# Performance work log

Measured on AMD Instinct MI355X. Metric: run time of the kernel, lower is better.

The kernel has to match this reference:

```python
import jax, jax.numpy as jnp
import numpy as np

DIM = 512
NUM_HEADS = 8
HEAD_DIM = DIM // NUM_HEADS
SCALE = HEAD_DIM ** -0.5
B, N = 8, 1024


def setup_inputs() -> dict:
    key = jax.random.key(0)
    k1, k2, k3, k4, k5 = jax.random.split(key, 5)
    x = jax.random.normal(k1, (B, N, DIM), dtype=jnp.float32)
    rpe_bias = jax.random.normal(k2, (1, NUM_HEADS, N, N), dtype=jnp.float32)
    # torch Linear weights: [out_features, in_features], y = x @ W.T
    qkv_w = jax.random.normal(k3, (3 * DIM, DIM), dtype=jnp.float32) * (DIM ** -0.5)
    proj_w = jax.random.normal(k4, (DIM, DIM), dtype=jnp.float32) * (DIM ** -0.5)
    proj_b = jax.random.normal(k5, (DIM,), dtype=jnp.float32) * 0.01
    return {"x": x, "rpe_bias": rpe_bias, "qkv_w": qkv_w, "proj_w": proj_w, "proj_b": proj_b}


def reference(x, rpe_bias, qkv_w, proj_w, proj_b):
    b, n, c = x.shape
    h, d = NUM_HEADS, HEAD_DIM
    # qkv projection (no bias): [B,N,3C] -> [3,B,H,N,D]
    qkv = (x @ qkv_w.T).reshape(b, n, 3, h, d).transpose(2, 0, 3, 1, 4)
    q, k, v = qkv[0], qkv[1], qkv[2]
    attn = jnp.einsum('bhnd,bhmd->bhnm', q, k) * SCALE + rpe_bias
    attn = jax.nn.softmax(attn, axis=-1)  # dropout p=0 -> identity
    out = jnp.einsum('bhnm,bhmd->bhnd', attn, v)
    out = out.transpose(0, 2, 1, 3).reshape(b, n, c)
    return out @ proj_w.T + proj_b
```

## Files before the change

### kernel.cpp

```cpp
#include <hip/hip_runtime.h>
#include <hip/hip_bf16.h>

#define B_    8
#define N_    1024
#define DIM_  512
#define H_    8
#define DH_   64
#define SCALE_ 0.125f

typedef unsigned short u16;
typedef __attribute__((ext_vector_type(8))) short bf16x8;
typedef __attribute__((ext_vector_type(4))) float f32x4;

__device__ __forceinline__ u16 f2bf(float f) {
  union { float f; unsigned u; } v; v.f = f;
  return (u16)((v.u + 0x7fffu + ((v.u >> 16) & 1u)) >> 16);
}
__device__ __forceinline__ unsigned pack2(float a, float b) {
  return (unsigned)f2bf(a) | ((unsigned)f2bf(b) << 16);
}
__device__ __forceinline__ void cp16(const void* g, void* l) {
  __builtin_amdgcn_global_load_lds(
      (const __attribute__((address_space(1))) unsigned*)g,
      (__attribute__((address_space(3))) unsigned*)l, 16, 0, 0);
}

__global__ __launch_bounds__(256) void convert_kernel(
    const float* __restrict__ X, const float* __restrict__ Wq,
    const float* __restrict__ Wp, u16* __restrict__ Xb,
    u16* __restrict__ Wqb, u16* __restrict__ Wpb) {
  const int NX4 = (B_ * N_ * DIM_) / 4;
  const int NQ4 = (3 * DIM_ * DIM_) / 4;
  const int NP4 = (DIM_ * DIM_) / 4;
  const int total = NX4 + NQ4 + NP4;
  const int stride = gridDim.x * 256;
  for (int i = blockIdx.x * 256 + threadIdx.x; i < total; i += stride) {
    const float* s; u16* d; int off;
    if (i < NX4)            { s = X;  d = Xb;  off = i; }
    else if (i < NX4 + NQ4) { s = Wq; d = Wqb; off = i - NX4; }
    else                    { s = Wp; d = Wpb; off = i - NX4 - NQ4; }
    float4 f = *(const float4*)(s + (size_t)off * 4);
    uint2 u; u.x = pack2(f.x, f.y); u.y = pack2(f.z, f.w);
    *(uint2*)(d + (size_t)off * 4) = u;
  }
}

__global__ __launch_bounds__(256) void qkv_gemm(
    const u16* __restrict__ Ab, const u16* __restrict__ Bb,
    u16* __restrict__ Q, u16* __restrict__ K, u16* __restrict__ Vt) {
  __shared__ __align__(16) u16 sA[128 * 64];
  __shared__ __align__(16) u16 sB[128 * 64];
  const int t = threadIdx.x;
  const int wv = t >> 6, lane = t & 63, quad = (lane >> 4) & 3, l15 = lane & 15;
  const int wr = wv >> 1, wc = wv & 1;
  const int m0 = blockIdx.y * 128;
  const int n0 = blockIdx.x * 128;

  const int srow = lane >> 3;
  const int schunk = (lane & 7) ^ srow;
  const size_t ga = (size_t)(m0 + srow) * DIM_ + schunk * 8;
  const size_t gb = (size_t)(n0 + srow) * DIM_ + schunk * 8;

  f32x4 zero = {0.f, 0.f, 0.f, 0.f};
  f32x4 acc[4][4];
#pragma unroll
  for (int i = 0; i < 4; i++)
#pragma unroll
    for (int j = 0; j < 4; j++) acc[i][j] = zero;

  for (int k0 = 0; k0 < DIM_; k0 += 64) {
    __syncthreads();
#pragma unroll
    for (int i = 0; i < 4; i++) {
      const int rb = 32 * wv + 8 * i;
      cp16(Ab + ga + (size_t)rb * DIM_ + k0, &sA[rb * 64]);
      cp16(Bb + gb + (size_t)rb * DIM_ + k0, &sB[rb * 64]);
    }
    __syncthreads();
#pragma unroll
    for (int ks = 0; ks < 2; ks++) {
      bf16x8 af[4], bfv[4];
#pragma unroll
      for (int i = 0; i < 4; i++)
        af[i] = *(const bf16x8*)&sA[(wr * 64 + 16 * i + l15) * 64 +
                                    (((ks << 2) | quad) ^ (l15 & 7)) * 8];
#pragma unroll
      for (int j = 0; j < 4; j++)
        bfv[j] = *(const bf16x8*)&sB[(wc * 64 + 16 * j + l15) * 64 +
                                     (((ks << 2) | quad) ^ (l15 & 7)) * 8];
#pragma unroll
      for (int i = 0; i < 4; i++)
#pragma unroll
        for (int j = 0; j < 4; j++)
          acc[i][j] = __builtin_amdgcn_mfma_f32_16x16x32_bf16(af[i], bfv[j], acc[i][j], 0, 0, 0);
    }
  }

  const int tsel = n0 >> 9;
#pragma unroll
  for (int j = 0; j < 4; j++) {
    const int jg = n0 + wc * 64 + 16 * j + l15;
    const int h = (jg >> 6) & 7, d = jg & 63;
#pragma unroll
    for (int i = 0; i < 4; i++) {
      const int mbase = m0 + wr * 64 + 16 * i + quad * 4;
      const int b = mbase >> 10, nb = mbase & 1023;
      const size_t bh = (size_t)(b * H_ + h);
      if (tsel == 2) {
        ushort4 v4;
        v4.x = f2bf(acc[i][j][0]); v4.y = f2bf(acc[i][j][1]);
        v4.z = f2bf(acc[i][j][2]); v4.w = f2bf(acc[i][j][3]);
        *(ushort4*)&Vt[(bh * DH_ + d) * N_ + nb] = v4;
      } else {
        u16* dst = (tsel == 0 ? Q : K);
#pragma unroll
        for (int rr = 0; rr < 4; rr++)
          dst[(bh * N_ + nb + rr) * DH_ + d] = f2bf(acc[i][j][rr]);
      }
    }
  }
}

__global__ __launch_bounds__(256) void attn_kernel(
    const u16* __restrict__ Q, const u16* __restrict__ K,
    const u16* __restrict__ Vt, const float* __restrict__ bias,
    u16* __restrict__ AO) {
  __shared__ __align__(16) u16 sK[64 * 72];
  __shared__ __align__(16) u16 sV[64 * 72];
  __shared__ __align__(16) u16 sP[64 * 72];
  const int t = threadIdx.x;
  const int wv = t >> 6, lane = t & 63, quad = (lane >> 4) & 3, l15 = lane & 15;
  const int n0 = blockIdx.x * 64;
  const int bh = blockIdx.y;
  const int b = bh >> 3, h = bh & 7;
  const int r = t >> 2, c = (t & 3) << 4;

  const int qg = n0 + 16 * wv + l15;
  bf16x8 qf0, qf1;
  {
    const u16* qsrc = Q + (((size_t)bh << 10) + qg) * DH_ + (quad << 3);
    qf0 = *(const bf16x8*)qsrc;
    qf1 = *(const bf16x8*)(qsrc + 32);
  }

  const float* bp = bias + (((size_t)h << 10) + qg) * N_ + (quad << 2);
  const u16* kbase = K + (((size_t)bh << 10) + r) * DH_ + c;
  const u16* vbase = Vt + (((size_t)bh << 6) + r) * N_ + c;

  f32x4 zero = {0.f, 0.f, 0.f, 0.f};
  f32x4 O[4];
  O[0] = zero; O[1] = zero; O[2] = zero; O[3] = zero;
  float lsum = 0.f;

  uint4 ka = *(const uint4*)kbase, kb2 = *(const uint4*)(kbase + 8);
  uint4 va = *(const uint4*)vbase, vb2 = *(const uint4*)(vbase + 8);
  float4 bias4[4];
#pragma unroll
  for (int cb = 0; cb < 4; cb++) bias4[cb] = *(const float4*)(bp + 16 * cb);

  for (int kt = 0; kt < 16; kt++) {
    __syncthreads();
    *(uint4*)&sK[r * 72 + c] = ka;  *(uint4*)&sK[r * 72 + c + 8] = kb2;
    *(uint4*)&sV[r * 72 + c] = va;  *(uint4*)&sV[r * 72 + c + 8] = vb2;
    if (kt < 15) {
      const u16* kn = kbase + (size_t)(kt + 1) * 64 * DH_;
      const u16* vn = vbase + (kt + 1) * 64;
      ka = *(const uint4*)kn; kb2 = *(const uint4*)(kn + 8);
      va = *(const uint4*)vn; vb2 = *(const uint4*)(vn + 8);
    }
    __syncthreads();

    f32x4 S[4];
    S[0] = zero; S[1] = zero; S[2] = zero; S[3] = zero;
#pragma unroll
    for (int ks = 0; ks < 2; ks++) {
      const bf16x8 qf = ks ? qf1 : qf0;
#pragma unroll
      for (int cb = 0; cb < 4; cb++) {
        bf16x8 kf = *(const bf16x8*)&sK[(16 * cb + l15) * 72 + ks * 32 + (quad << 3)];
        S[cb] = __builtin_amdgcn_mfma_f32_16x16x32_bf16(kf, qf, S[cb], 0, 0, 0);
      }
    }

#pragma unroll
    for (int cb = 0; cb < 4; cb++) {
      float p0 = __expf(fmaf(S[cb][0], SCALE_, bias4[cb].x));
      float p1 = __expf(fmaf(S[cb][1], SCALE_, bias4[cb].y));
      float p2 = __expf(fmaf(S[cb][2], SCALE_, bias4[cb].z));
      float p3 = __expf(fmaf(S[cb][3], SCALE_, bias4[cb].w));
      lsum += (p0 + p1) + (p2 + p3);
      uint2 pk;
      pk.x = pack2(p0, p1);
      pk.y = pack2(p2, p3);
      *(uint2*)&sP[(16 * wv + l15) * 72 + 16 * cb + (quad << 2)] = pk;
    }
    if (kt < 15) {
      const float* bn = bp + (kt + 1) * 64;
#pragma unroll
      for (int cb = 0; cb < 4; cb++) bias4[cb] = *(const float4*)(bn + 16 * cb);
    }
    asm volatile("s_waitcnt lgkmcnt(0)" ::: "memory");

#pragma unroll
    for (int ks = 0; ks < 2; ks++) {
      bf16x8 pf = *(const bf16x8*)&sP[(16 * wv + l15) * 72 + ks * 32 + (quad << 3)];
#pragma unroll
      for (int cb = 0; cb < 4; cb++) {
        bf16x8 vf = *(const bf16x8*)&sV[(16 * cb + l15) * 72 + ks * 32 + (quad << 3)];
        O[cb] = __builtin_amdgcn_mfma_f32_16x16x32_bf16(vf, pf, O[cb], 0, 0, 0);
      }
    }
  }

  lsum += __shfl_xor(lsum, 16);
  lsum += __shfl_xor(lsum, 32);
  const float inv = 1.f / lsum;
#pragma unroll
  for (int cb = 0; cb < 4; cb++) {
    ushort4 o4;
    o4.x = f2bf(O[cb][0] * inv); o4.y = f2bf(O[cb][1] * inv);
    o4.z = f2bf(O[cb][2] * inv); o4.w = f2bf(O[cb][3] * inv);
    *(ushort4*)&AO[(((size_t)b << 10) + qg) * DIM_ + h * DH_ + 16 * cb + (quad << 2)] = o4;
  }
}

__global__ __launch_bounds__(256) void proj_gemm(
    const u16* __restrict__ Ab, const u16* __restrict__ Bb,
    const float* __restrict__ Pb, float* __restrict__ Out) {
  __shared__ __align__(16) u16 sA[128 * 64];
  __shared__ __align__(16) u16 sB[128 * 64];
  const int t = threadIdx.x;
  const int wv = t >> 6, lane = t & 63, quad = (lane >> 4) & 3, l15 = lane & 15;
  const int wr = wv >> 1, wc = wv & 1;
  const int m0 = blockIdx.y * 128;
  const int n0 = blockIdx.x * 128;

  const int srow = lane >> 3;
  const int schunk = (lane & 7) ^ srow;
  const size_t ga = (size_t)(m0 + srow) * DIM_ + schunk * 8;
  const size_t gb = (size_t)(n0 + srow) * DIM_ + schunk * 8;

  f32x4 zero = {0.f, 0.f, 0.f, 0.f};
  f32x4 acc[4][4];
#pragma unroll
  for (int i = 0; i < 4; i++)
#pragma unroll
    for (int j = 0; j < 4; j++) acc[i][j] = zero;

  for (int k0 = 0; k0 < DIM_; k0 += 64) {
    __syncthreads();
#pragma unroll
    for (int i = 0; i < 4; i++) {
      const int rb = 32 * wv + 8 * i;
      cp16(Ab + ga + (size_t)rb * DIM_ + k0, &sA[rb * 64]);
      cp16(Bb + gb + (size_t)rb * DIM_ + k0, &sB[rb * 64]);
    }
    __syncthreads();
#pragma unroll
    for (int ks = 0; ks < 2; ks++) {
      bf16x8 af[4], bfv[4];
#pragma unroll
      for (int i = 0; i < 4; i++)
        af[i] = *(const bf16x8*)&sA[(wr * 64 + 16 * i + l15) * 64 +
                                    (((ks << 2) | quad) ^ (l15 & 7)) * 8];
#pragma unroll
      for (int j = 0; j < 4; j++)
        bfv[j] = *(const bf16x8*)&sB[(wc * 64 + 16 * j + l15) * 64 +
                                     (((ks << 2) | quad) ^ (l15 & 7)) * 8];
#pragma unroll
      for (int i = 0; i < 4; i++)
#pragma unroll
        for (int j = 0; j < 4; j++)
          acc[i][j] = __builtin_amdgcn_mfma_f32_16x16x32_bf16(af[i], bfv[j], acc[i][j], 0, 0, 0);
    }
  }

#pragma unroll
  for (int j = 0; j < 4; j++) {
    const int jg = n0 + wc * 64 + 16 * j + l15;
    const float pb = Pb[jg];
#pragma unroll
    for (int i = 0; i < 4; i++) {
      const int mbase = m0 + wr * 64 + 16 * i + quad * 4;
#pragma unroll
      for (int rr = 0; rr < 4; rr++)
        Out[(size_t)(mbase + rr) * DIM_ + jg] = acc[i][j][rr] + pb;
    }
  }
}

extern "C" void kernel_launch(void* const* d_in, const int* in_sizes, int n_in,
                              void* d_out, int out_size, void* d_ws, size_t ws_size,
                              hipStream_t stream) {
  const float* x      = (const float*)d_in[0];
  const float* rpe    = (const float*)d_in[1];
  const float* qkv_w  = (const float*)d_in[2];
  const float* proj_w = (const float*)d_in[3];
  const float* proj_b = (const float*)d_in[4];
  float* out = (float*)d_out;

  const size_t perbuf = (size_t)B_ * N_ * DIM_;
  u16* Xb  = (u16*)d_ws;
  u16* Q   = Xb + perbuf;
  u16* K   = Q + perbuf;
  u16* Vt  = K + perbuf;
  u16* Wqb = Vt + perbuf;
  u16* Wpb = Wqb + (size_t)3 * DIM_ * DIM_;
  u16* AO  = Xb;

  convert_kernel<<<2560, 256, 0, stream>>>(x, qkv_w, proj_w, Xb, Wqb, Wpb);
  qkv_gemm<<<dim3(12, 64), 256, 0, stream>>>(Xb, Wqb, Q, K, Vt);
  attn_kernel<<<dim3(16, 64), 256, 0, stream>>>(Q, K, Vt, rpe, AO);
  proj_gemm<<<dim3(4, 64), 256, 0, stream>>>(AO, Wpb, proj_b, out);
}
```

Before: 176.6 us.

## Double-buffer K/V/bias prefetch in attention and remap block order for bias reuse

The attention loop now keeps two register sets for K, V and bias tiles, prefetching two tiles ahead so global load latency has more compute to hide behind. The grid changes to a 1D launch where the head index varies fastest and batch next. Consecutive blocks then share the same rpe_bias rows across batches, which should improve L2 reuse of the large bias tensor. The deeper prefetch roughly doubles the prefetch registers, which may reduce occupancy.

```diff
diff --git a/kernel.cpp b/kernel.cpp
--- a/kernel.cpp
+++ b/kernel.cpp
@@ -130,9 +130,14 @@
   __shared__ __align__(16) u16 sP[64 * 72];
   const int t = threadIdx.x;
   const int wv = t >> 6, lane = t & 63, quad = (lane >> 4) & 3, l15 = lane & 15;
-  const int n0 = blockIdx.x * 64;
-  const int bh = blockIdx.y;
-  const int b = bh >> 3, h = bh & 7;
+
+  const int bid = blockIdx.x;
+  const int h = bid & 7;
+  const int s = bid >> 3;
+  const int nx = s >> 3;
+  const int b = s & 7;
+  const int n0 = nx * 64;
+  const int bh = b * H_ + h;
   const int r = t >> 2, c = (t & 3) << 4;
 
   const int qg = n0 + 16 * wv + l15;
@@ -152,21 +157,28 @@
   O[0] = zero; O[1] = zero; O[2] = zero; O[3] = zero;
   float lsum = 0.f;
 
-  uint4 ka = *(const uint4*)kbase, kb2 = *(const uint4*)(kbase + 8);
-  uint4 va = *(const uint4*)vbase, vb2 = *(const uint4*)(vbase + 8);
-  float4 bias4[4];
-#pragma unroll
-  for (int cb = 0; cb < 4; cb++) bias4[cb] = *(const float4*)(bp + 16 * cb);
-
-  for (int kt = 0; kt < 16; kt++) {
-    __syncthreads();
-    *(uint4*)&sK[r * 72 + c] = ka;  *(uint4*)&sK[r * 72 + c + 8] = kb2;
-    *(uint4*)&sV[r * 72 + c] = va;  *(uint4*)&sV[r * 72 + c + 8] = vb2;
-    if (kt < 15) {
-      const u16* kn = kbase + (size_t)(kt + 1) * 64 * DH_;
-      const u16* vn = vbase + (kt + 1) * 64;
-      ka = *(const uint4*)kn; kb2 = *(const uint4*)(kn + 8);
-      va = *(const uint4*)vn; vb2 = *(const uint4*)(vn + 8);
+  uint4 kA0 = *(const uint4*)kbase, kA1 = *(const uint4*)(kbase + 8);
+  uint4 vA0 = *(const uint4*)vbase, vA1 = *(const uint4*)(vbase + 8);
+  uint4 kB0 = *(const uint4*)(kbase + (size_t)64 * DH_);
+  uint4 kB1 = *(const uint4*)(kbase + (size_t)64 * DH_ + 8);
+  uint4 vB0 = *(const uint4*)(vbase + 64), vB1 = *(const uint4*)(vbase + 72);
+  float4 bA[4], bB[4];
+#pragma unroll
+  for (int cb = 0; cb < 4; cb++) {
+    bA[cb] = *(const float4*)(bp + 16 * cb);
+    bB[cb] = *(const float4*)(bp + 64 + 16 * cb);
+  }
+
+  auto tile = [&](int kt, uint4& k0r, uint4& k1r, uint4& v0r, uint4& v1r,
+                  float4 (&bias4)[4]) {
+    __syncthreads();
+    *(uint4*)&sK[r * 72 + c] = k0r;  *(uint4*)&sK[r * 72 + c + 8] = k1r;
+    *(uint4*)&sV[r * 72 + c] = v0r;  *(uint4*)&sV[r * 72 + c + 8] = v1r;
+    if (kt + 2 < 16) {
+      const u16* kn = kbase + (size_t)(kt + 2) * 64 * DH_;
+      const u16* vn = vbase + (kt + 2) * 64;
+      k0r = *(const uint4*)kn; k1r = *(const uint4*)(kn + 8);
+      v0r = *(const uint4*)vn; v1r = *(const uint4*)(vn + 8);
     }
     __syncthreads();
 
@@ -194,8 +206,8 @@
       pk.y = pack2(p2, p3);
       *(uint2*)&sP[(16 * wv + l15) * 72 + 16 * cb + (quad << 2)] = pk;
     }
-    if (kt < 15) {
-      const float* bn = bp + (kt + 1) * 64;
+    if (kt + 2 < 16) {
+      const float* bn = bp + (kt + 2) * 64;
 #pragma unroll
       for (int cb = 0; cb < 4; cb++) bias4[cb] = *(const float4*)(bn + 16 * cb);
     }
@@ -210,6 +222,11 @@
         O[cb] = __builtin_amdgcn_mfma_f32_16x16x32_bf16(vf, pf, O[cb], 0, 0, 0);
       }
     }
+  };
+
+  for (int kt = 0; kt < 16; kt += 2) {
+    tile(kt, kA0, kA1, vA0, vA1, bA);
+    tile(kt + 1, kB0, kB1, vB0, vB1, bB);
   }
 
   lsum += __shfl_xor(lsum, 16);
@@ -310,6 +327,6 @@
 
   convert_kernel<<<2560, 256, 0, stream>>>(x, qkv_w, proj_w, Xb, Wqb, Wpb);
   qkv_gemm<<<dim3(12, 64), 256, 0, stream>>>(Xb, Wqb, Q, K, Vt);
-  attn_kernel<<<dim3(16, 64), 256, 0, stream>>>(Q, K, Vt, rpe, AO);
+  attn_kernel<<<1024, 256, 0, stream>>>(Q, K, Vt, rpe, AO);
   proj_gemm<<<dim3(4, 64), 256, 0, stream>>>(AO, Wpb, proj_b, out);
 }
```

Measured after the change: 182.2 us. +3.2%, slower.
